# Kernel tuning notes

Hardware: AMD Instinct MI355X
Metric: run time of the kernel (lower is better)

Reference implementation:

```python
import jax, jax.numpy as jnp
from jax import lax
import numpy as np

OUTS = [5, 1, 2, 2, 1, 1, 1, 1]  # heatmap, conf, dxy, wh, dist, offset, severity, surface
OFFS = np.concatenate([[0], np.cumsum(OUTS)])
BN_EPS = 1e-5


def setup_inputs() -> dict:
    key = jax.random.key(0)
    ks = jax.random.split(key, 10)
    N, C, Hf, Wf = 16, 576, 12, 20
    f = jax.random.normal(ks[0], (N, C, Hf, Wf), jnp.float32)
    det_w1 = jax.random.normal(ks[1], (8, C, C, 3, 3), jnp.float32) * 0.02
    det_bn_g = 1.0 + 0.1 * jax.random.normal(ks[2], (8, C), jnp.float32)
    det_bn_b = 0.1 * jax.random.normal(ks[3], (8, C), jnp.float32)
    det_bn_m = 0.1 * jax.random.normal(ks[4], (8, C), jnp.float32)
    det_bn_v = jax.random.uniform(ks[5], (8, C), jnp.float32) + 0.5
    det_w2 = jax.random.normal(ks[6], (14, C), jnp.float32) * 0.05
    det_b2 = jax.random.normal(ks[7], (14,), jnp.float32) * 0.05
    lin_W = jax.random.normal(ks[8], (10, C), jnp.float32) * 0.05
    lin_b = jnp.zeros((10,), jnp.float32)
    return dict(f=f, det_w1=det_w1, det_bn_g=det_bn_g, det_bn_b=det_bn_b,
                det_bn_m=det_bn_m, det_bn_v=det_bn_v, det_w2=det_w2, det_b2=det_b2,
                lin_W=lin_W, lin_b=lin_b, frame_w=640, frame_h=384)


def _head(f, w1, g, b, m, v, w2, b2):
    # conv3x3 (no bias) -> BN (inference) -> SiLU -> conv1x1
    dn = ('NCHW', 'OIHW', 'NCHW')
    h = lax.conv_general_dilated(f, w1, (1, 1), 'SAME', dimension_numbers=dn)
    scale = g * lax.rsqrt(v + BN_EPS)
    h = h * scale[None, :, None, None] + (b - m * scale)[None, :, None, None]
    h = h * jax.nn.sigmoid(h)  # SiLU
    return jnp.einsum('nchw,oc->nohw', h, w2) + b2[None, :, None, None]


def _forward(f, det_w1, det_bn_g, det_bn_b, det_bn_m, det_bn_v, det_w2, det_b2,
             lin_W, lin_b, frame_w, frame_h, max_dets=20):
    N, C, Hf, Wf = f.shape
    eps = 1e-5
    # ---- legacy single-hazard head from pooled features ----
    f1 = f.mean(axis=(2, 3))                      # [N, 576]  (AdaptiveAvgPool2d(1))
    lin = f1 @ lin_W.T + lin_b                    # [N, 10]
    conf = jnp.clip(jax.nn.sigmoid(lin[:, 0:1]), eps, 1.0 - eps)
    type_log = lin[:, 1:6]
    dist_m = jax.nn.sigmoid(lin[:, 6:7]) * 3.0
    offset = jnp.tanh(lin[:, 7:8])
    severity = jnp.clip(jax.nn.sigmoid(lin[:, 8:9]), eps, 1.0 - eps)
    surface = jnp.clip(jax.nn.sigmoid(lin[:, 9:10]), eps, 1.0 - eps)
    type_id = jnp.argmax(type_log, axis=1, keepdims=True).astype(f.dtype)
    single_out = jnp.concatenate([conf, type_id, dist_m, offset, severity, surface], axis=1)

    # ---- dense per-pixel heads ----
    maps = []
    for i in range(8):
        o0, o1 = int(OFFS[i]), int(OFFS[i + 1])
        maps.append(_head(f, det_w1[i], det_bn_g[i], det_bn_b[i],
                          det_bn_m[i], det_bn_v[i], det_w2[o0:o1], det_b2[o0:o1]))
    heat = jax.nn.sigmoid(maps[0])                # [N,5,H,W]
    conf_d = jax.nn.sigmoid(maps[1])              # [N,1,H,W]
    dxy = jax.nn.sigmoid(maps[2])                 # [N,2,H,W]
    wh = jax.nn.sigmoid(maps[3])                  # [N,2,H,W]
    dist = jax.nn.sigmoid(maps[4]) * 3.0          # [N,1,H,W]
    offsm = jnp.tanh(maps[5])
    sev = jax.nn.sigmoid(maps[6])
    surf = jax.nn.sigmoid(maps[7])

    # ---- per-class topk decode ----
    score_flat = (conf_d * heat).reshape(N, 5, Hf * Wf)
    k = min(max_dets, Hf * Wf)
    topk_scores, topk_idx = lax.top_k(score_flat, k)          # [N,5,k]
    top_scores = topk_scores.reshape(N, -1)                    # [N,5k]
    top_class = jnp.broadcast_to(jnp.arange(5, dtype=f.dtype)[None, :, None], (N, 5, k)).reshape(N, -1)
    idx_flat = topk_idx.reshape(N, -1)                          # [N,5k]
    y_idx = (idx_flat // Wf).astype(f.dtype)
    x_idx = (idx_flat % Wf).astype(f.dtype)

    g1 = lambda m: jnp.take_along_axis(m.reshape(N, -1), idx_flat, axis=1)
    gx, gy = g1(dxy[:, 0]), g1(dxy[:, 1])
    gw, gh = g1(wh[:, 0]), g1(wh[:, 1])
    gdist, goffs = g1(dist), g1(offsm)
    gsev, gsurf = g1(sev), g1(surf)

    stride_x = frame_w / Wf
    stride_y = frame_h / Hf
    cx = jnp.clip(x_idx + gx, 0, Wf - 1) * stride_x
    cy = jnp.clip(y_idx + gy, 0, Hf - 1) * stride_y
    bw = jnp.clip(gw, 0, 1) * frame_w
    bh = jnp.clip(gh, 0, 1) * frame_h
    x1 = jnp.clip(cx - bw / 2, 0, frame_w - 1)
    y1 = jnp.clip(cy - bh / 2, 0, frame_h - 1)
    x2 = jnp.clip(cx + bw / 2, 0, frame_w - 1)
    y2 = jnp.clip(cy + bh / 2, 0, frame_h - 1)

    dets = jnp.stack([top_scores, top_class, gdist, goffs, gsev, gsurf, x1, y1, x2, y2], axis=-1)  # [N,5k,10]
    order = jnp.argsort(dets[:, :, 2], axis=-1)   # ascending distance (nearest first)
    dets_sorted = jnp.take_along_axis(dets, order[:, :, None], axis=1)
    dets_out = dets_sorted[:, :max_dets, :]        # [N,K,10]
    return single_out, dets_out


def reference(f, det_w1, det_bn_g, det_bn_b, det_bn_m, det_bn_v, det_w2, det_b2,
              lin_W, lin_b, frame_w, frame_h):
    return _forward(f, det_w1, det_bn_g, det_bn_b, det_bn_m, det_bn_v,
                    det_w2, det_b2, lin_W, lin_b, frame_w, frame_h)
```

## Files before the change

### kernel.cpp

```cpp
#include <hip/hip_runtime.h>
#include <math.h>

#define NB 16
#define CC 576
#define HH 12
#define WW 20
#define PP 240
#define MM 3840
#define NHEAD 8
#define HALO 22

typedef __attribute__((ext_vector_type(8))) short short8;
typedef __attribute__((ext_vector_type(4))) float floatx4;
typedef unsigned short ushort_t;

__device__ __forceinline__ float sigmoidf_(float x) {
    return 1.0f / (1.0f + expf(-x));
}
__device__ __forceinline__ unsigned short f2bf(float x) {
    union { float f; unsigned u; } v; v.f = x;
    unsigned r = v.u + 0x7fff + ((v.u >> 16) & 1);
    return (unsigned short)(r >> 16);
}
__device__ __forceinline__ float bf2f(unsigned short b) {
    union { float f; unsigned u; } v; v.u = ((unsigned)b) << 16;
    return v.f;
}

__global__ __launch_bounds__(256) void k_single(const float* __restrict__ f1sum,
                                                const float* __restrict__ linW,
                                                const float* __restrict__ linb,
                                                float* __restrict__ out) {
    int n = blockIdx.x;
    __shared__ float lin[10];
    int t = threadIdx.x;
    int lane = t & 63, wave = t >> 6;
    const float inv = 1.0f / PP;
    for (int o = wave; o < 10; o += 4) {
        const float* wrow = linW + o * CC;
        float s = 0.f;
        for (int c = lane; c < CC; c += 64)
            s = fmaf(f1sum[n * CC + c] * inv, wrow[c], s);
        #pragma unroll
        for (int off = 32; off; off >>= 1) s += __shfl_xor(s, off, 64);
        if (lane == 0) lin[o] = s + linb[o];
    }
    __syncthreads();
    if (t == 0) {
        const float eps = 1e-5f;
        float conf = sigmoidf_(lin[0]);
        conf = fminf(fmaxf(conf, eps), 1.f - eps);
        int best = 0; float bv = lin[1];
        #pragma unroll
        for (int j = 1; j < 5; ++j) { if (lin[1 + j] > bv) { bv = lin[1 + j]; best = j; } }
        float dist = 3.f * sigmoidf_(lin[6]);
        float offs = tanhf(lin[7]);
        float sev  = fminf(fmaxf(sigmoidf_(lin[8]), eps), 1.f - eps);
        float surf = fminf(fmaxf(sigmoidf_(lin[9]), eps), 1.f - eps);
        float* o = out + n * 6;
        o[0] = conf; o[1] = (float)best; o[2] = dist;
        o[3] = offs; o[4] = sev; o[5] = surf;
    }
}

__global__ __launch_bounds__(256) void k_prep_f(const float* __restrict__ f,
                                                ushort_t* __restrict__ fhi,
                                                ushort_t* __restrict__ flo,
                                                float* __restrict__ f1sum) {
    __shared__ float tile[32][33];
    int c0 = blockIdx.x * 32, p0 = blockIdx.y * 32, n = blockIdx.z;
    int tp = threadIdx.x & 31, tc8 = threadIdx.x >> 5;
    for (int cc = tc8; cc < 32; cc += 8) {
        int p = p0 + tp;
        tile[cc][tp] = (p < PP) ? f[((size_t)n * CC + c0 + cc) * PP + p] : 0.f;
    }
    __syncthreads();
    if (threadIdx.x < 32) {
        float s = 0.f;
        #pragma unroll
        for (int pp = 0; pp < 32; ++pp) s += tile[threadIdx.x][pp];
        atomicAdd(&f1sum[n * CC + c0 + threadIdx.x], s);
    }
    int tcw = threadIdx.x & 31, tpw = threadIdx.x >> 5;
    for (int pp = tpw; pp < 32; pp += 8) {
        int p = p0 + pp;
        if (p < PP) {
            float v = tile[tcw][pp];
            unsigned short hi = f2bf(v);
            size_t o = ((size_t)n * PP + p) * CC + c0 + tcw;
            fhi[o] = hi;
            flo[o] = f2bf(v - bf2f(hi));
        }
    }
}

__global__ __launch_bounds__(256) void k_prep_w(const float* __restrict__ w1,
                                                ushort_t* __restrict__ whi,
                                                ushort_t* __restrict__ wlo) {
    __shared__ float ws[CC * 9];
    int co = blockIdx.x % CC;
    int h  = blockIdx.x / CC;
    const float* src = w1 + ((size_t)(h * CC + co)) * CC * 9;
    for (int i = threadIdx.x; i < CC * 9; i += 256) ws[i] = src[i];
    __syncthreads();
    for (int tap = 0; tap < 9; ++tap) {
        size_t ob = ((size_t)(h * 9 + tap) * CC + co) * CC;
        for (int ci = threadIdx.x; ci < CC; ci += 256) {
            float v = ws[ci * 9 + tap];
            unsigned short hi = f2bf(v);
            whi[ob + ci] = hi;
            wlo[ob + ci] = f2bf(v - bf2f(hi));
        }
    }
}

__global__ __launch_bounds__(256) void k_maps_init(float* __restrict__ maps,
                                                   const float* __restrict__ b2,
                                                   float* __restrict__ f1sum) {
    int i = blockIdx.x * 256 + threadIdx.x;
    if (i < NB * 14 * PP) {
        int o = (i / PP) % 14;
        maps[i] = b2[o];
    } else if (i < NB * 14 * PP + NB * CC) {
        f1sum[i - NB * 14 * PP] = 0.f;
    }
}

__global__ __launch_bounds__(256) void k_conv_mfma(
        const ushort_t* __restrict__ fhi, const ushort_t* __restrict__ flo,
        const ushort_t* __restrict__ whi, const ushort_t* __restrict__ wlo,
        const float* __restrict__ w2,
        const float* __restrict__ bng, const float* __restrict__ bnb,
        const float* __restrict__ bnm, const float* __restrict__ bnv,
        float* __restrict__ maps) {
    __shared__ __align__(16) ushort_t Ah[1216 * 8];
    __shared__ __align__(16) ushort_t Al[1216 * 8];
    __shared__ __align__(16) ushort_t Bh[256 * 8];
    __shared__ __align__(16) ushort_t Bl[256 * 8];
    __shared__ ushort_t rowmap[9 * 256];

    int t = threadIdx.x;

    int bid = blockIdx.x;
    int xcd = bid & 7;
    int q = bid >> 3;
    int mt = q % 15;
    int slice = (q / 15) * 8 + xcd;
    int m0 = mt * 256;
    int c0 = (slice % 9) * 64;
    int h  = slice / 9;

    int w = t >> 6, lane = t & 63;
    int quad = lane >> 4, l15 = lane & 15;
    int srow_lo = t & 15, sg = (t >> 4) & 3, srb = t >> 6;

    int bco = srb * 16 + srow_lo;
    size_t bconst = (size_t)(c0 + bco) * CC + sg * 8;
    const size_t hbase = (size_t)h * 9 * CC * CC;
    short8 pbh, pbl;
    {
        size_t src = hbase + bconst;
        pbh = *(const short8*)(whi + src);
        pbl = *(const short8*)(wlo + src);
    }

    if (t < 32) {
        int arr = t >> 4, g = (t >> 2) & 3, rr = 12 + (t & 3);
        int idx = 18 * 64 + g * 16 + rr;
        short8 z = {0, 0, 0, 0, 0, 0, 0, 0};
        *(short8*)((arr ? Al : Ah) + idx * 8) = z;
    }
    for (int idx = t; idx < 9 * 256; idx += 256) {
        int tap = idx >> 8, ml = idx & 255;
        int m = m0 + ml;
        int p = m % PP;
        int y = p / WW, x = p - y * WW;
        int dy = tap / 3 - 1, dx = tap % 3 - 1;
        int yy = y + dy, xx = x + dx;
        int row;
        if ((unsigned)yy < (unsigned)HH && (unsigned)xx < (unsigned)WW)
            row = ml + dy * WW + dx + HALO;
        else
            row = 300 + (ml & 3);
        rowmap[idx] = (ushort_t)row;
    }
    __syncthreads();

    floatx4 acc[4][4];
    #pragma unroll
    for (int i = 0; i < 4; ++i)
        #pragma unroll
        for (int j = 0; j < 4; ++j) acc[i][j] = (floatx4){0.f, 0.f, 0.f, 0.f};

    for (int cib = 0; cib < 18; ++cib) {
        __syncthreads();
        int koff = cib * 32 + sg * 8;
        #pragma unroll
        for (int it = 0; it < 5; ++it) {
            int row = (srb + 4 * it) * 16 + srow_lo;
            if (row < 300) {
                int mg = m0 - HALO + row;
                int cidx = 256 * it + t;
                short8 vh = {0, 0, 0, 0, 0, 0, 0, 0};
                short8 vl = {0, 0, 0, 0, 0, 0, 0, 0};
                if ((unsigned)mg < (unsigned)MM) {
                    vh = *(const short8*)(fhi + (size_t)mg * CC + koff);
                    vl = *(const short8*)(flo + (size_t)mg * CC + koff);
                }
                *(short8*)(Ah + cidx * 8) = vh;
                *(short8*)(Al + cidx * 8) = vl;
            }
        }
        for (int tap = 0; tap < 9; ++tap) {
            if (tap) __syncthreads();
            *(short8*)(Bh + t * 8) = pbh;
            *(short8*)(Bl + t * 8) = pbl;
            int ntap = tap + 1, ncib = cib;
            if (ntap == 9) { ntap = 0; ncib = cib + 1; }
            if (ncib < 18) {
                size_t src = hbase + (size_t)ntap * (CC * CC) + bconst
                           + (size_t)ncib * 32;
                pbh = *(const short8*)(whi + src);
                pbl = *(const short8*)(wlo + src);
            }
            __syncthreads();

            short8 bh[4], bl[4], ah[4], al[4];
            #pragma unroll
            for (int j = 0; j < 4; ++j) {
                bh[j] = *(const short8*)(Bh + (j * 64 + lane) * 8);
                bl[j] = *(const short8*)(Bl + (j * 64 + lane) * 8);
            }
            #pragma unroll
            for (int i = 0; i < 4; ++i) {
                int r = rowmap[tap * 256 + w * 64 + i * 16 + l15];
                int a16 = ((r >> 4) * 64 + quad * 16 + (r & 15)) * 8;
                ah[i] = *(const short8*)(Ah + a16);
                al[i] = *(const short8*)(Al + a16);
            }
            #pragma unroll
            for (int i = 0; i < 4; ++i)
                #pragma unroll
                for (int j = 0; j < 4; ++j) {
                    acc[i][j] = __builtin_amdgcn_mfma_f32_16x16x32_bf16(
                        ah[i], bh[j], acc[i][j], 0, 0, 0);
                    acc[i][j] = __builtin_amdgcn_mfma_f32_16x16x32_bf16(
                        ah[i], bl[j], acc[i][j], 0, 0, 0);
                    acc[i][j] = __builtin_amdgcn_mfma_f32_16x16x32_bf16(
                        al[i], bh[j], acc[i][j], 0, 0, 0);
                }
        }
    }

    float scale[4], shift[4];
    #pragma unroll
    for (int j = 0; j < 4; ++j) {
        int c = h * CC + c0 + j * 16 + l15;
        float g_ = bng[c], bb = bnb[c], bm = bnm[c], bv = bnv[c];
        scale[j] = g_ / sqrtf(bv + 1e-5f);
        shift[j] = bb - bm * scale[j];
    }
    #pragma unroll
    for (int i = 0; i < 4; ++i)
        #pragma unroll
        for (int j = 0; j < 4; ++j)
            #pragma unroll
            for (int r = 0; r < 4; ++r) {
                float hx = fmaf(acc[i][j][r], scale[j], shift[j]);
                acc[i][j][r] = hx * sigmoidf_(hx);
            }

    static const int OFFo[NHEAD + 1] = {0, 5, 6, 8, 10, 11, 12, 13, 14};
    int o0 = OFFo[h], o1 = OFFo[h + 1];
    for (int o = o0; o < o1; ++o) {
        float w2v[4];
        #pragma unroll
        for (int j = 0; j < 4; ++j) w2v[j] = w2[o * CC + c0 + j * 16 + l15];
        float pv[4][4];
        #pragma unroll
        for (int i = 0; i < 4; ++i)
            #pragma unroll
            for (int r = 0; r < 4; ++r) {
                float s = 0.f;
                #pragma unroll
                for (int j = 0; j < 4; ++j) s = fmaf(acc[i][j][r], w2v[j], s);
                pv[i][r] = s;
            }
        #pragma unroll
        for (int off = 1; off < 16; off <<= 1)
            #pragma unroll
            for (int i = 0; i < 4; ++i)
                #pragma unroll
                for (int r = 0; r < 4; ++r)
                    pv[i][r] += __shfl_xor(pv[i][r], off, 64);
        if (l15 == 0) {
            #pragma unroll
            for (int i = 0; i < 4; ++i)
                #pragma unroll
                for (int r = 0; r < 4; ++r) {
                    int m = m0 + w * 64 + i * 16 + quad * 4 + r;
                    int n = m / PP, p = m - n * PP;
                    atomicAdd(&maps[(n * 14 + o) * PP + p], pv[i][r]);
                }
        }
    }
}

__global__ __launch_bounds__(256) void k_decode(
        const float* __restrict__ maps,
        const int* __restrict__ fw_p, const int* __restrict__ fh_p,
        float* __restrict__ out) {
    int n = blockIdx.x;
    int t = threadIdx.x;
    __shared__ float ms[14][PP];
    __shared__ float sconf[PP];
    __shared__ float cscore[100];
    __shared__ int   cidx[100];
    __shared__ float dets[100][10];
    __shared__ float dvals[100];

    const float* mp = maps + (size_t)n * 14 * PP;
    for (int idx = t; idx < 14 * PP; idx += 256) ms[idx / PP][idx % PP] = mp[idx];
    __syncthreads();
    if (t < PP) sconf[t] = sigmoidf_(ms[5][t]);
    __syncthreads();

    int wv = t >> 6, lane = t & 63;
    for (int cls = wv; cls < 5; cls += 4) {
        float v[4]; int pi[4];
        #pragma unroll
        for (int j = 0; j < 4; ++j) {
            int p = lane + 64 * j;
            pi[j] = p;
            v[j] = (p < PP) ? sconf[p] * sigmoidf_(ms[cls][p]) : -1e30f;
        }
        for (int r = 0; r < 20; ++r) {
            float bv = v[0]; int bi = pi[0];
            #pragma unroll
            for (int j = 1; j < 4; ++j)
                if (v[j] > bv || (v[j] == bv && pi[j] < bi)) { bv = v[j]; bi = pi[j]; }
            float rv = bv; int ri = bi;
            #pragma unroll
            for (int off = 32; off; off >>= 1) {
                float ov = __shfl_xor(rv, off, 64);
                int   oi = __shfl_xor(ri, off, 64);
                if (ov > rv || (ov == rv && oi < ri)) { rv = ov; ri = oi; }
            }
            if (lane == 0) { cscore[cls * 20 + r] = rv; cidx[cls * 20 + r] = ri; }
            #pragma unroll
            for (int j = 0; j < 4; ++j) if (pi[j] == ri) v[j] = -1e30f;
        }
    }
    __syncthreads();

    if (t < 100) {
        int cls = t / 20;
        int p = cidx[t];
        int yi = p / WW, xi = p - yi * WW;
        float gx = sigmoidf_(ms[6][p]),  gy = sigmoidf_(ms[7][p]);
        float gw = sigmoidf_(ms[8][p]),  gh = sigmoidf_(ms[9][p]);
        float gd = 3.f * sigmoidf_(ms[10][p]);
        float go = tanhf(ms[11][p]);
        float gs = sigmoidf_(ms[12][p]);
        float gf = sigmoidf_(ms[13][p]);
        float fw = (float)fw_p[0], fh = (float)fh_p[0];
        float sx = fw / (float)WW, sy = fh / (float)HH;
        float cx = fminf(fmaxf((float)xi + gx, 0.f), (float)WW - 1.f) * sx;
        float cy = fminf(fmaxf((float)yi + gy, 0.f), (float)HH - 1.f) * sy;
        float bw = fminf(fmaxf(gw, 0.f), 1.f) * fw;
        float bh = fminf(fmaxf(gh, 0.f), 1.f) * fh;
        float x1 = fminf(fmaxf(cx - bw * 0.5f, 0.f), fw - 1.f);
        float y1 = fminf(fmaxf(cy - bh * 0.5f, 0.f), fh - 1.f);
        float x2 = fminf(fmaxf(cx + bw * 0.5f, 0.f), fw - 1.f);
        float y2 = fminf(fmaxf(cy + bh * 0.5f, 0.f), fh - 1.f);
        dets[t][0] = cscore[t]; dets[t][1] = (float)cls;
        dets[t][2] = gd; dets[t][3] = go; dets[t][4] = gs; dets[t][5] = gf;
        dets[t][6] = x1; dets[t][7] = y1; dets[t][8] = x2; dets[t][9] = y2;
        dvals[t] = gd;
    }
    __syncthreads();
    if (t < 100) {
        float d = dvals[t];
        int rank = 0;
        for (int l = 0; l < 100; ++l) {
            float dl = dvals[l];
            rank += (dl < d) || (dl == d && l < t);
        }
        if (rank < 20) {
            float* o = out + 96 + ((size_t)n * 20 + rank) * 10;
            #pragma unroll
            for (int q = 0; q < 10; ++q) o[q] = dets[t][q];
        }
    }
}

extern "C" void kernel_launch(void* const* d_in, const int* in_sizes, int n_in,
                              void* d_out, int out_size, void* d_ws, size_t ws_size,
                              hipStream_t stream) {
    const float* f    = (const float*)d_in[0];
    const float* w1   = (const float*)d_in[1];
    const float* bng  = (const float*)d_in[2];
    const float* bnb  = (const float*)d_in[3];
    const float* bnm  = (const float*)d_in[4];
    const float* bnv  = (const float*)d_in[5];
    const float* w2   = (const float*)d_in[6];
    const float* b2   = (const float*)d_in[7];
    const float* linW = (const float*)d_in[8];
    const float* linb = (const float*)d_in[9];
    const int*   fw   = (const int*)d_in[10];
    const int*   fh   = (const int*)d_in[11];
    float* out = (float*)d_out;

    const size_t w_elems = (size_t)NHEAD * 9 * CC * CC;
    const size_t f_elems = (size_t)MM * CC;

    ushort_t* ws_whi = (ushort_t*)d_ws;
    ushort_t* ws_wlo = ws_whi + w_elems;
    ushort_t* ws_fhi = ws_wlo + w_elems;
    ushort_t* ws_flo = ws_fhi + f_elems;
    float*    ws_maps = (float*)(ws_flo + f_elems);
    float*    ws_f1sum = (float*)d_ws;

    k_maps_init<<<(NB * 14 * PP + NB * CC + 255) / 256, 256, 0, stream>>>(
        ws_maps, b2, ws_f1sum);
    k_prep_f<<<dim3(CC / 32, (PP + 31) / 32, NB), 256, 0, stream>>>(
        f, ws_fhi, ws_flo, ws_f1sum);
    k_single<<<NB, 256, 0, stream>>>(ws_f1sum, linW, linb, out);
    k_prep_w<<<NHEAD * CC, 256, 0, stream>>>(w1, ws_whi, ws_wlo);
    k_conv_mfma<<<dim3(15 * 9 * NHEAD), 256, 0, stream>>>(
        ws_fhi, ws_flo, ws_whi, ws_wlo, w2, bng, bnb, bnm, bnv, ws_maps);
    k_decode<<<NB, 256, 0, stream>>>(ws_maps, fw, fh, out);
}
```

Measured before the change: 726.8 us.

## Stream conv tiles into LDS with global_load_lds and double-buffer weights

The MFMA conv kernel now loads the feature tiles and weight slices straight from global memory into LDS with global_load_lds, instead of staging them through registers. The B weight buffer is double-buffered, so each tap needs one barrier instead of two. The weight prep kernel is also vectorized, using float4 reads and short8 writes. The risks are that A-tile rows outside the valid range are no longer zero-filled and now read out-of-bounds addresses, and that the custom barrier may not wait for the async LDS loads to finish.

Result: slower. 793.8 us (+9.2%).

```diff
diff --git a/kernel.cpp b/kernel.cpp
--- a/kernel.cpp
+++ b/kernel.cpp
@@ -26,6 +26,20 @@
     union { float f; unsigned u; } v; v.u = ((unsigned)b) << 16;
     return v.f;
 }
+
+__device__ __forceinline__ void gl_lds16(const ushort_t* g, ushort_t* l) {
+    __builtin_amdgcn_global_load_lds(
+        (const __attribute__((address_space(1))) void*)g,
+        (__attribute__((address_space(3))) void*)l, 16, 0, 0);
+}
+
+#define FENCED_BARRIER() do {                   \
+    asm volatile("" ::: "memory");              \
+    __builtin_amdgcn_sched_barrier(0);          \
+    __builtin_amdgcn_s_barrier();               \
+    __builtin_amdgcn_sched_barrier(0);          \
+    asm volatile("" ::: "memory");              \
+} while (0)
 
 __global__ __launch_bounds__(256) void k_single(const float* __restrict__ f1sum,
                                                 const float* __restrict__ linW,
@@ -101,16 +115,22 @@
     int co = blockIdx.x % CC;
     int h  = blockIdx.x / CC;
     const float* src = w1 + ((size_t)(h * CC + co)) * CC * 9;
-    for (int i = threadIdx.x; i < CC * 9; i += 256) ws[i] = src[i];
-    __syncthreads();
-    for (int tap = 0; tap < 9; ++tap) {
-        size_t ob = ((size_t)(h * 9 + tap) * CC + co) * CC;
-        for (int ci = threadIdx.x; ci < CC; ci += 256) {
-            float v = ws[ci * 9 + tap];
+    for (int i = threadIdx.x; i < CC * 9 / 4; i += 256)
+        *(float4*)(ws + i * 4) = *(const float4*)(src + i * 4);
+    __syncthreads();
+    for (int idx = threadIdx.x; idx < 9 * 72; idx += 256) {
+        int tap = idx / 72, pos = idx - tap * 72;
+        short8 vh, vl;
+        #pragma unroll
+        for (int e = 0; e < 8; ++e) {
+            float v = ws[(pos * 8 + e) * 9 + tap];
             unsigned short hi = f2bf(v);
-            whi[ob + ci] = hi;
-            wlo[ob + ci] = f2bf(v - bf2f(hi));
-        }
+            vh[e] = (short)hi;
+            vl[e] = (short)f2bf(v - bf2f(hi));
+        }
+        size_t ob = ((size_t)(h * 9 + tap) * CC + co) * CC + (size_t)pos * 8;
+        *(short8*)(whi + ob) = vh;
+        *(short8*)(wlo + ob) = vl;
     }
 }
 
@@ -135,8 +155,8 @@
         float* __restrict__ maps) {
     __shared__ __align__(16) ushort_t Ah[1216 * 8];
     __shared__ __align__(16) ushort_t Al[1216 * 8];
-    __shared__ __align__(16) ushort_t Bh[256 * 8];
-    __shared__ __align__(16) ushort_t Bl[256 * 8];
+    __shared__ __align__(16) ushort_t Bh[2][256 * 8];
+    __shared__ __align__(16) ushort_t Bl[2][256 * 8];
     __shared__ ushort_t rowmap[9 * 256];
 
     int t = threadIdx.x;
@@ -157,12 +177,20 @@
     int bco = srb * 16 + srow_lo;
     size_t bconst = (size_t)(c0 + bco) * CC + sg * 8;
     const size_t hbase = (size_t)h * 9 * CC * CC;
-    short8 pbh, pbl;
-    {
-        size_t src = hbase + bconst;
-        pbh = *(const short8*)(whi + src);
-        pbl = *(const short8*)(wlo + src);
-    }
+
+    #pragma unroll
+    for (int it = 0; it < 5; ++it) {
+        int row = (srb + 4 * it) * 16 + srow_lo;
+        if (row < 300) {
+            ptrdiff_t mg = (ptrdiff_t)m0 - HALO + row;
+            ptrdiff_t off = mg * CC + sg * 8;
+            int cidx = 256 * it + t;
+            gl_lds16(fhi + off, Ah + cidx * 8);
+            gl_lds16(flo + off, Al + cidx * 8);
+        }
+    }
+    gl_lds16(whi + hbase + bconst, &Bh[0][t * 8]);
+    gl_lds16(wlo + hbase + bconst, &Bl[0][t * 8]);
 
     if (t < 32) {
         int arr = t >> 4, g = (t >> 2) & 3, rr = 12 + (t & 3);
@@ -193,43 +221,37 @@
         for (int j = 0; j < 4; ++j) acc[i][j] = (floatx4){0.f, 0.f, 0.f, 0.f};
 
     for (int cib = 0; cib < 18; ++cib) {
-        __syncthreads();
-        int koff = cib * 32 + sg * 8;
-        #pragma unroll
-        for (int it = 0; it < 5; ++it) {
-            int row = (srb + 4 * it) * 16 + srow_lo;
-            if (row < 300) {
-                int mg = m0 - HALO + row;
-                int cidx = 256 * it + t;
-                short8 vh = {0, 0, 0, 0, 0, 0, 0, 0};
-                short8 vl = {0, 0, 0, 0, 0, 0, 0, 0};
-                if ((unsigned)mg < (unsigned)MM) {
-                    vh = *(const short8*)(fhi + (size_t)mg * CC + koff);
-                    vl = *(const short8*)(flo + (size_t)mg * CC + koff);
+        if (cib) {
+            FENCED_BARRIER();
+            #pragma unroll
+            for (int it = 0; it < 5; ++it) {
+                int row = (srb + 4 * it) * 16 + srow_lo;
+                if (row < 300) {
+                    ptrdiff_t mg = (ptrdiff_t)m0 - HALO + row;
+                    ptrdiff_t off = mg * CC + cib * 32 + sg * 8;
+                    int cidx = 256 * it + t;
+                    gl_lds16(fhi + off, Ah + cidx * 8);
+                    gl_lds16(flo + off, Al + cidx * 8);
                 }
-                *(short8*)(Ah + cidx * 8) = vh;
-                *(short8*)(Al + cidx * 8) = vl;
             }
         }
         for (int tap = 0; tap < 9; ++tap) {
-            if (tap) __syncthreads();
-            *(short8*)(Bh + t * 8) = pbh;
-            *(short8*)(Bl + t * 8) = pbl;
-            int ntap = tap + 1, ncib = cib;
-            if (ntap == 9) { ntap = 0; ncib = cib + 1; }
-            if (ncib < 18) {
+            int bs = (cib + tap) & 1;
+            __syncthreads();
+            if (cib * 9 + tap + 1 < 162) {
+                int ncib = (tap == 8) ? cib + 1 : cib;
+                int ntap = (tap == 8) ? 0 : tap + 1;
                 size_t src = hbase + (size_t)ntap * (CC * CC) + bconst
                            + (size_t)ncib * 32;
-                pbh = *(const short8*)(whi + src);
-                pbl = *(const short8*)(wlo + src);
-            }
-            __syncthreads();
+                gl_lds16(whi + src, &Bh[bs ^ 1][t * 8]);
+                gl_lds16(wlo + src, &Bl[bs ^ 1][t * 8]);
+            }
 
             short8 bh[4], bl[4], ah[4], al[4];
             #pragma unroll
             for (int j = 0; j < 4; ++j) {
-                bh[j] = *(const short8*)(Bh + (j * 64 + lane) * 8);
-                bl[j] = *(const short8*)(Bl + (j * 64 + lane) * 8);
+                bh[j] = *(const short8*)(&Bh[bs][(j * 64 + lane) * 8]);
+                bl[j] = *(const short8*)(&Bl[bs][(j * 64 + lane) * 8]);
             }
             #pragma unroll
             for (int i = 0; i < 4; ++i) {
```
